# Performance work log

Measured on AMD Instinct MI355X. Metric: run time of the kernel, lower is better.

The kernel has to match this reference:

```python
import jax, jax.numpy as jnp
import numpy as np

NEG_BIG = -9e15  # matches torch's -9000000000000000.0 masked-fill value
ALPHA = 0.2      # LeakyReLU negative slope


def setup_inputs() -> dict:
    key = jax.random.key(0)
    k1, k2, k3, k4 = jax.random.split(key, 4)
    N, F_in, F_out = 8192, 128, 64
    h = jax.random.normal(k1, (N, F_in), dtype=jnp.float32)
    adj = jax.random.randint(k2, (N, N), 0, 2).astype(jnp.float32)
    # Glorot(gain=1.414)-scale params
    W = jax.random.normal(k3, (F_in, F_out), dtype=jnp.float32) * (1.414 * np.sqrt(2.0 / (F_in + F_out)))
    a = jax.random.normal(k4, (2 * F_out, 1), dtype=jnp.float32) * (1.414 * np.sqrt(2.0 / (2 * F_out + 1)))
    return {"h": h, "adj": adj, "W": W, "a": a}


def reference(h, adj, W, a):
    F_out = W.shape[1]
    Wh = h @ W                               # [N, F_out]
    Wh1 = Wh @ a[:F_out, :]                  # [N, 1]
    Wh2 = Wh @ a[F_out:, :]                  # [N, 1]
    e = jax.nn.leaky_relu(Wh1 + Wh2.T, negative_slope=ALPHA)  # [N, N]
    attention = jnp.where(adj > 0, e, NEG_BIG)
    attention = jax.nn.softmax(attention, axis=1)
    # dropout omitted (eval mode / p applied only in training)
    h_prime = attention @ Wh                 # [N, F_out]
    return jax.nn.elu(h_prime)               # concat=True -> ELU
```

## Files before the change

### kernel.cpp

```cpp
#include <hip/hip_runtime.h>
#include <hip/hip_bf16.h>

#define N 8192
#define FIN 128
#define FOUT 64
#define ALPHA 0.2f
#define LOG2E 1.44269504f
#define JSPAN N
#define STJ 256
#define NST (JSPAN / STJ)

typedef __attribute__((ext_vector_type(8))) short short8;
typedef __attribute__((ext_vector_type(4))) float f32x4;

static __device__ __forceinline__ unsigned fkey(float x) {
    unsigned u = __float_as_uint(x);
    return (u >> 31) ? ~u : (u | 0x80000000u);
}
static __device__ __forceinline__ float fdecode(unsigned k) {
    unsigned u = (k & 0x80000000u) ? (k & 0x7FFFFFFFu) : ~k;
    return __uint_as_float(u);
}
static __device__ __forceinline__ void gll16(const float* g, float* l) {
    __builtin_amdgcn_global_load_lds(
        (const __attribute__((address_space(1))) unsigned int*)g,
        (__attribute__((address_space(3))) unsigned int*)l, 16, 0, 0);
}

__global__ __launch_bounds__(256) void k_prep(const float* __restrict__ h,
                                              const float* __restrict__ W,
                                              const float* __restrict__ a,
                                              float* __restrict__ Wh,
                                              float* __restrict__ s2,
                                              float* __restrict__ t2,
                                              unsigned* __restrict__ keys) {
    __shared__ float lH[16 * FIN];
    __shared__ float lW[FIN * FOUT];
    __shared__ float red[8];
    const int tid = threadIdx.x;
    const int r0 = blockIdx.x * 16;
    {
        const float4* src = (const float4*)(h + (size_t)r0 * FIN);
        float4* dst = (float4*)lH;
        for (int i = tid; i < 16 * FIN / 4; i += 256) dst[i] = src[i];
        const float4* ws_ = (const float4*)W;
        float4* dw = (float4*)lW;
        for (int i = tid; i < FIN * FOUT / 4; i += 256) dw[i] = ws_[i];
    }
    __syncthreads();
    const int wave = tid >> 6, lane = tid & 63;
    float acc[4] = {0.f, 0.f, 0.f, 0.f};
    for (int k = 0; k < FIN; ++k) {
        float wv = lW[k * FOUT + lane];
#pragma unroll
        for (int r = 0; r < 4; ++r)
            acc[r] = fmaf(lH[(wave * 4 + r) * FIN + k], wv, acc[r]);
    }
    const float a1 = a[lane], a2 = a[FOUT + lane];
    float smx = -1e30f, tmx = -1e30f;
#pragma unroll
    for (int r = 0; r < 4; ++r) {
        int row = r0 + wave * 4 + r;
        Wh[(size_t)row * FOUT + lane] = acc[r];
        float sv = acc[r] * a1, tv = acc[r] * a2;
#pragma unroll
        for (int off = 32; off; off >>= 1) {
            sv += __shfl_xor(sv, off);
            tv += __shfl_xor(tv, off);
        }
        sv *= LOG2E; tv *= LOG2E;
        if (lane == 0) { s2[row] = sv; t2[row] = tv; }
        smx = fmaxf(smx, sv);
        tmx = fmaxf(tmx, tv);
    }
    if (lane == 0) { red[wave] = smx; red[4 + wave] = tmx; }
    __syncthreads();
    if (tid == 0) {
        float ms = fmaxf(fmaxf(red[0], red[1]), fmaxf(red[2], red[3]));
        float mt = fmaxf(fmaxf(red[4], red[5]), fmaxf(red[6], red[7]));
        atomicMax(keys + 0, fkey(ms));
        atomicMax(keys + 1, fkey(mt));
    }
}

__global__ __launch_bounds__(256) void k_pack(const float* __restrict__ Wh,
                                              __hip_bfloat16* __restrict__ WhB) {
    const int c = blockIdx.x;
    const int tn = threadIdx.x >> 6;
    const int lane = threadIdx.x & 63;
    const int quad = lane >> 4, l16 = lane & 15;
    const float* src = Wh + ((size_t)(c * 32 + quad * 8)) * FOUT + tn * 16 + l16;
    union { unsigned short u[8]; short8 v; } frag;
#pragma unroll
    for (int e = 0; e < 8; ++e) {
        __hip_bfloat16 b = __float2bfloat16(src[(size_t)e * FOUT]);
        frag.u[e] = *(unsigned short*)&b;
    }
    *(short8*)&WhB[(((size_t)c * 4 + tn) * 64 + lane) * 8] = frag.v;
}

__global__ __launch_bounds__(256) void k_attn(const float* __restrict__ adj,
                                              const __hip_bfloat16* __restrict__ WhB,
                                              const float* __restrict__ s2,
                                              const float* __restrict__ t2,
                                              const unsigned* __restrict__ keys,
                                              float* __restrict__ out) {
    __shared__ float bufA[2][8 * 512];
    __shared__ float tl[JSPAN];
    __shared__ float sred[64];
    const int wave = threadIdx.x >> 6, lane = threadIdx.x & 63;
    const int quad = lane >> 4, l16 = lane & 15;
    const int i0 = blockIdx.x * 16;
    const int u0 = 2 * wave;

    const float* gaw = adj + (size_t)(i0 + l16) * N + quad * 8;
    gll16(gaw + u0 * 32,      &bufA[0][u0 * 512]);
    gll16(gaw + u0 * 32 + 4,  &bufA[0][u0 * 512 + 256]);
    gll16(gaw + u0 * 32 + 32, &bufA[0][(u0 + 1) * 512]);
    gll16(gaw + u0 * 32 + 36, &bufA[0][(u0 + 1) * 512 + 256]);

    {
        const float4* src = (const float4*)t2;
        float4* dst = (float4*)tl;
        for (int i = threadIdx.x; i < JSPAN / 4; i += 256) dst[i] = src[i];
    }
    const float mraw = fdecode(keys[0]) + fdecode(keys[1]);
    const float mm = mraw > 0.f ? mraw : ALPHA * mraw;
    const float sm = s2[i0 + l16];
    const short8* BF = (const short8*)WhB;

    f32x4 acc0 = {0,0,0,0}, acc1 = {0,0,0,0}, acc2 = {0,0,0,0}, acc3 = {0,0,0,0};
    float lsum = 0.f;
    __syncthreads();

    for (int st = 0; st < NST; ++st) {
        const int b = st & 1;
        const size_t kc = (size_t)(st * 8 + u0) * 4;
        short8 B00 = BF[(kc + 0) * 64 + lane];
        short8 B01 = BF[(kc + 1) * 64 + lane];
        short8 B02 = BF[(kc + 2) * 64 + lane];
        short8 B03 = BF[(kc + 3) * 64 + lane];
        short8 B10 = BF[(kc + 4) * 64 + lane];
        short8 B11 = BF[(kc + 5) * 64 + lane];
        short8 B12 = BF[(kc + 6) * 64 + lane];
        short8 B13 = BF[(kc + 7) * 64 + lane];
        __builtin_amdgcn_sched_barrier(0);
        if (st + 1 < NST) {
            const float* g = gaw + (st + 1) * STJ + u0 * 32;
            float* d = &bufA[b ^ 1][u0 * 512];
            gll16(g, d);
            gll16(g + 4, d + 256);
            gll16(g + 32, d + 512);
            gll16(g + 36, d + 768);
            __builtin_amdgcn_sched_barrier(0);
            asm volatile("s_waitcnt vmcnt(12)" ::: "memory");
        } else {
            asm volatile("s_waitcnt vmcnt(8)" ::: "memory");
        }
        __builtin_amdgcn_sched_barrier(0);
#pragma unroll
        for (int uu = 0; uu < 2; ++uu) {
            const int ul = u0 + uu;
            const float* Au = &bufA[b][ul * 512];
            float4 alo = *(const float4*)(Au + lane * 4);
            float4 ahi = *(const float4*)(Au + 256 + lane * 4);
            const float* Tp = tl + st * STJ + ul * 32 + quad * 8;
            float4 tlo = *(const float4*)Tp;
            float4 thi = *(const float4*)(Tp + 4);
            union { __hip_bfloat162 h2[4]; short8 v; } af;
#pragma unroll
            for (int pp = 0; pp < 4; ++pp) {
                float a0 = (pp < 2) ? ((const float*)&alo)[2 * pp]     : ((const float*)&ahi)[2 * pp - 4];
                float a1 = (pp < 2) ? ((const float*)&alo)[2 * pp + 1] : ((const float*)&ahi)[2 * pp - 3];
                float t0 = (pp < 2) ? ((const float*)&tlo)[2 * pp]     : ((const float*)&thi)[2 * pp - 4];
                float t1 = (pp < 2) ? ((const float*)&tlo)[2 * pp + 1] : ((const float*)&thi)[2 * pp - 3];
                float x0 = sm + t0,                x1 = sm + t1;
                float le0 = fmaxf(x0, ALPHA * x0), le1 = fmaxf(x1, ALPHA * x1);
                float p0 = a0 * exp2f(le0 - mm),   p1 = a1 * exp2f(le1 - mm);
                __hip_bfloat162 pb = __float22bfloat162_rn(make_float2(p0, p1));
                af.h2[pp] = pb;
                lsum += __bfloat162float(pb.x) + __bfloat162float(pb.y);
            }
            if (uu == 0) {
                acc0 = __builtin_amdgcn_mfma_f32_16x16x32_bf16(af.v, B00, acc0, 0, 0, 0);
                acc1 = __builtin_amdgcn_mfma_f32_16x16x32_bf16(af.v, B01, acc1, 0, 0, 0);
                acc2 = __builtin_amdgcn_mfma_f32_16x16x32_bf16(af.v, B02, acc2, 0, 0, 0);
                acc3 = __builtin_amdgcn_mfma_f32_16x16x32_bf16(af.v, B03, acc3, 0, 0, 0);
            } else {
                acc0 = __builtin_amdgcn_mfma_f32_16x16x32_bf16(af.v, B10, acc0, 0, 0, 0);
                acc1 = __builtin_amdgcn_mfma_f32_16x16x32_bf16(af.v, B11, acc1, 0, 0, 0);
                acc2 = __builtin_amdgcn_mfma_f32_16x16x32_bf16(af.v, B12, acc2, 0, 0, 0);
                acc3 = __builtin_amdgcn_mfma_f32_16x16x32_bf16(af.v, B13, acc3, 0, 0, 0);
            }
        }
    }

    lsum += __shfl_xor(lsum, 16);
    lsum += __shfl_xor(lsum, 32);

    float* accr = &bufA[0][0];
    *(f32x4*)&accr[((wave * 4 + 0) * 64 + lane) * 4] = acc0;
    *(f32x4*)&accr[((wave * 4 + 1) * 64 + lane) * 4] = acc1;
    *(f32x4*)&accr[((wave * 4 + 2) * 64 + lane) * 4] = acc2;
    *(f32x4*)&accr[((wave * 4 + 3) * 64 + lane) * 4] = acc3;
    if (lane < 16) sred[wave * 16 + lane] = lsum;
    __syncthreads();

    const int tile = wave;
    f32x4 tot = {0, 0, 0, 0};
#pragma unroll
    for (int w = 0; w < 4; ++w) {
        f32x4 c = *(const f32x4*)&accr[((w * 4 + tile) * 64 + lane) * 4];
        tot[0] += c[0]; tot[1] += c[1]; tot[2] += c[2]; tot[3] += c[3];
    }
#pragma unroll
    for (int r = 0; r < 4; ++r) {
        int row = quad * 4 + r;
        float lv = sred[row] + sred[16 + row] + sred[32 + row] + sred[48 + row];
        float v = tot[r] / lv;
        out[(size_t)(i0 + row) * FOUT + tile * 16 + l16] =
            v > 0.f ? v : (exp2f(v * LOG2E) - 1.f);
    }
}

extern "C" void kernel_launch(void* const* d_in, const int* in_sizes, int n_in,
                              void* d_out, int out_size, void* d_ws, size_t ws_size,
                              hipStream_t stream) {
    const float* h   = (const float*)d_in[0];
    const float* adj = (const float*)d_in[1];
    const float* W   = (const float*)d_in[2];
    const float* a   = (const float*)d_in[3];
    float* out = (float*)d_out;

    char* base = (char*)d_ws;
    float* Wh = (float*)base;                        base += (size_t)N * FOUT * 4;
    __hip_bfloat16* WhB = (__hip_bfloat16*)base;     base += (size_t)N * FOUT * 2;
    float* s2 = (float*)base;                        base += (size_t)N * 4;
    float* t2 = (float*)base;                        base += (size_t)N * 4 + 1024;
    unsigned* keys = (unsigned*)base;

    hipMemsetAsync(keys, 0, 2 * sizeof(unsigned), stream);
    k_prep<<<N / 16, 256, 0, stream>>>(h, W, a, Wh, s2, t2, keys);
    k_pack<<<N / 32, 256, 0, stream>>>(Wh, WhB);
    k_attn<<<N / 16, 256, 0, stream>>>(adj, WhB, s2, t2, keys, out);
}
```

Before: 403.3 us.

## Fuse bf16 packing into prep and triple-buffer adj with register-prefetched B/t2

Folds the bf16 fragment packing of Wh into the prep kernel, so the separate pack launch and the fp32 Wh round trip through global memory go away. The attention kernel moves from double to triple buffering of adj tiles, issuing loads two stages ahead. It also prefetches the next stage's WhB fragments and t2 values into registers instead of staging all of t2 in LDS. This drops the LDS t2 copy and the startup __syncthreads, at the cost of more live registers and hand-tuned vmcnt waits that must match the issue order exactly.

Result: no change. 398.5 us (-1.2%).

```diff
diff --git a/kernel.cpp b/kernel.cpp
--- a/kernel.cpp
+++ b/kernel.cpp
@@ -6,9 +6,8 @@
 #define FOUT 64
 #define ALPHA 0.2f
 #define LOG2E 1.44269504f
-#define JSPAN N
 #define STJ 256
-#define NST (JSPAN / STJ)
+#define NST (N / STJ)
 
 typedef __attribute__((ext_vector_type(8))) short short8;
 typedef __attribute__((ext_vector_type(4))) float f32x4;
@@ -30,38 +29,47 @@
 __global__ __launch_bounds__(256) void k_prep(const float* __restrict__ h,
                                               const float* __restrict__ W,
                                               const float* __restrict__ a,
-                                              float* __restrict__ Wh,
+                                              __hip_bfloat16* __restrict__ WhB,
                                               float* __restrict__ s2,
                                               float* __restrict__ t2,
                                               unsigned* __restrict__ keys) {
-    __shared__ float lH[16 * FIN];
+    __shared__ float lH[32 * FIN];
     __shared__ float lW[FIN * FOUT];
     __shared__ float red[8];
     const int tid = threadIdx.x;
-    const int r0 = blockIdx.x * 16;
+    const int c = blockIdx.x;
+    const int r0 = c * 32;
     {
         const float4* src = (const float4*)(h + (size_t)r0 * FIN);
         float4* dst = (float4*)lH;
-        for (int i = tid; i < 16 * FIN / 4; i += 256) dst[i] = src[i];
+        for (int i = tid; i < 32 * FIN / 4; i += 256) dst[i] = src[i];
         const float4* ws_ = (const float4*)W;
         float4* dw = (float4*)lW;
         for (int i = tid; i < FIN * FOUT / 4; i += 256) dw[i] = ws_[i];
     }
     __syncthreads();
     const int wave = tid >> 6, lane = tid & 63;
-    float acc[4] = {0.f, 0.f, 0.f, 0.f};
+    float acc[8] = {0.f, 0.f, 0.f, 0.f, 0.f, 0.f, 0.f, 0.f};
+#pragma unroll 4
     for (int k = 0; k < FIN; ++k) {
         float wv = lW[k * FOUT + lane];
 #pragma unroll
-        for (int r = 0; r < 4; ++r)
-            acc[r] = fmaf(lH[(wave * 4 + r) * FIN + k], wv, acc[r]);
-    }
+        for (int r = 0; r < 8; ++r)
+            acc[r] = fmaf(lH[(wave * 8 + r) * FIN + k], wv, acc[r]);
+    }
+    union { unsigned short u[8]; short8 v; } frag;
+#pragma unroll
+    for (int e = 0; e < 8; ++e) {
+        __hip_bfloat16 b = __float2bfloat16(acc[e]);
+        frag.u[e] = *(unsigned short*)&b;
+    }
+    *(short8*)&WhB[(((size_t)c * 4 + (lane >> 4)) * 64 + (wave * 16 + (lane & 15))) * 8] = frag.v;
+
     const float a1 = a[lane], a2 = a[FOUT + lane];
     float smx = -1e30f, tmx = -1e30f;
 #pragma unroll
-    for (int r = 0; r < 4; ++r) {
-        int row = r0 + wave * 4 + r;
-        Wh[(size_t)row * FOUT + lane] = acc[r];
+    for (int r = 0; r < 8; ++r) {
+        int row = r0 + wave * 8 + r;
         float sv = acc[r] * a1, tv = acc[r] * a2;
 #pragma unroll
         for (int off = 32; off; off >>= 1) {
@@ -83,90 +91,100 @@
     }
 }
 
-__global__ __launch_bounds__(256) void k_pack(const float* __restrict__ Wh,
-                                              __hip_bfloat16* __restrict__ WhB) {
-    const int c = blockIdx.x;
-    const int tn = threadIdx.x >> 6;
-    const int lane = threadIdx.x & 63;
-    const int quad = lane >> 4, l16 = lane & 15;
-    const float* src = Wh + ((size_t)(c * 32 + quad * 8)) * FOUT + tn * 16 + l16;
-    union { unsigned short u[8]; short8 v; } frag;
-#pragma unroll
-    for (int e = 0; e < 8; ++e) {
-        __hip_bfloat16 b = __float2bfloat16(src[(size_t)e * FOUT]);
-        frag.u[e] = *(unsigned short*)&b;
-    }
-    *(short8*)&WhB[(((size_t)c * 4 + tn) * 64 + lane) * 8] = frag.v;
-}
-
 __global__ __launch_bounds__(256) void k_attn(const float* __restrict__ adj,
                                               const __hip_bfloat16* __restrict__ WhB,
                                               const float* __restrict__ s2,
                                               const float* __restrict__ t2,
                                               const unsigned* __restrict__ keys,
                                               float* __restrict__ out) {
-    __shared__ float bufA[2][8 * 512];
-    __shared__ float tl[JSPAN];
+    __shared__ float bufA[3][8 * 512];
     __shared__ float sred[64];
     const int wave = threadIdx.x >> 6, lane = threadIdx.x & 63;
     const int quad = lane >> 4, l16 = lane & 15;
     const int i0 = blockIdx.x * 16;
     const int u0 = 2 * wave;
 
-    const float* gaw = adj + (size_t)(i0 + l16) * N + quad * 8;
-    gll16(gaw + u0 * 32,      &bufA[0][u0 * 512]);
-    gll16(gaw + u0 * 32 + 4,  &bufA[0][u0 * 512 + 256]);
-    gll16(gaw + u0 * 32 + 32, &bufA[0][(u0 + 1) * 512]);
-    gll16(gaw + u0 * 32 + 36, &bufA[0][(u0 + 1) * 512 + 256]);
-
-    {
-        const float4* src = (const float4*)t2;
-        float4* dst = (float4*)tl;
-        for (int i = threadIdx.x; i < JSPAN / 4; i += 256) dst[i] = src[i];
-    }
+    const float sm = s2[i0 + l16];
     const float mraw = fdecode(keys[0]) + fdecode(keys[1]);
     const float mm = mraw > 0.f ? mraw : ALPHA * mraw;
-    const float sm = s2[i0 + l16];
+    asm volatile("" :: "v"(sm), "v"(mm));
+    __builtin_amdgcn_sched_barrier(0);
+
+    const float* gawu = adj + (size_t)(i0 + l16) * N + quad * 8 + u0 * 32;
     const short8* BF = (const short8*)WhB;
+
+    gll16(gawu,      &bufA[0][u0 * 512]);
+    gll16(gawu + 4,  &bufA[0][u0 * 512 + 256]);
+    gll16(gawu + 32, &bufA[0][(u0 + 1) * 512]);
+    gll16(gawu + 36, &bufA[0][(u0 + 1) * 512 + 256]);
+    __builtin_amdgcn_sched_barrier(0);
+    size_t kc = (size_t)u0 * 4;
+    short8 B0 = BF[(kc + 0) * 64 + lane];
+    short8 B1 = BF[(kc + 1) * 64 + lane];
+    short8 B2 = BF[(kc + 2) * 64 + lane];
+    short8 B3 = BF[(kc + 3) * 64 + lane];
+    short8 B4 = BF[(kc + 4) * 64 + lane];
+    short8 B5 = BF[(kc + 5) * 64 + lane];
+    short8 B6 = BF[(kc + 6) * 64 + lane];
+    short8 B7 = BF[(kc + 7) * 64 + lane];
+    const float* Tp = t2 + u0 * 32 + quad * 8;
+    float4 T0 = *(const float4*)Tp;
+    float4 T1 = *(const float4*)(Tp + 4);
+    float4 T2v = *(const float4*)(Tp + 32);
+    float4 T3v = *(const float4*)(Tp + 36);
+    __builtin_amdgcn_sched_barrier(0);
+    gll16(gawu + STJ,      &bufA[1][u0 * 512]);
+    gll16(gawu + STJ + 4,  &bufA[1][u0 * 512 + 256]);
+    gll16(gawu + STJ + 32, &bufA[1][(u0 + 1) * 512]);
+    gll16(gawu + STJ + 36, &bufA[1][(u0 + 1) * 512 + 256]);
+    __builtin_amdgcn_sched_barrier(0);
 
     f32x4 acc0 = {0,0,0,0}, acc1 = {0,0,0,0}, acc2 = {0,0,0,0}, acc3 = {0,0,0,0};
     float lsum = 0.f;
-    __syncthreads();
+    int bi = 0;
 
     for (int st = 0; st < NST; ++st) {
-        const int b = st & 1;
-        const size_t kc = (size_t)(st * 8 + u0) * 4;
-        short8 B00 = BF[(kc + 0) * 64 + lane];
-        short8 B01 = BF[(kc + 1) * 64 + lane];
-        short8 B02 = BF[(kc + 2) * 64 + lane];
-        short8 B03 = BF[(kc + 3) * 64 + lane];
-        short8 B10 = BF[(kc + 4) * 64 + lane];
-        short8 B11 = BF[(kc + 5) * 64 + lane];
-        short8 B12 = BF[(kc + 6) * 64 + lane];
-        short8 B13 = BF[(kc + 7) * 64 + lane];
+        const bool hasN = (st + 1 < NST);
+        short8 nB0, nB1, nB2, nB3, nB4, nB5, nB6, nB7;
+        float4 nT0, nT1, nT2, nT3;
+        if (hasN) {
+            const size_t nkc = (size_t)((st + 1) * 8 + u0) * 4;
+            nB0 = BF[(nkc + 0) * 64 + lane];
+            nB1 = BF[(nkc + 1) * 64 + lane];
+            nB2 = BF[(nkc + 2) * 64 + lane];
+            nB3 = BF[(nkc + 3) * 64 + lane];
+            nB4 = BF[(nkc + 4) * 64 + lane];
+            nB5 = BF[(nkc + 5) * 64 + lane];
+            nB6 = BF[(nkc + 6) * 64 + lane];
+            nB7 = BF[(nkc + 7) * 64 + lane];
+            const float* nTp = t2 + (st + 1) * STJ + u0 * 32 + quad * 8;
+            nT0 = *(const float4*)nTp;
+            nT1 = *(const float4*)(nTp + 4);
+            nT2 = *(const float4*)(nTp + 32);
+            nT3 = *(const float4*)(nTp + 36);
+        }
         __builtin_amdgcn_sched_barrier(0);
-        if (st + 1 < NST) {
-            const float* g = gaw + (st + 1) * STJ + u0 * 32;
-            float* d = &bufA[b ^ 1][u0 * 512];
+        if (st + 2 < NST) {
+            const float* g = gawu + (st + 2) * STJ;
+            const int di = bi >= 1 ? bi - 1 : 2;
+            float* d = &bufA[di][u0 * 512];
             gll16(g, d);
             gll16(g + 4, d + 256);
             gll16(g + 32, d + 512);
             gll16(g + 36, d + 768);
-            __builtin_amdgcn_sched_barrier(0);
-            asm volatile("s_waitcnt vmcnt(12)" ::: "memory");
-        } else {
-            asm volatile("s_waitcnt vmcnt(8)" ::: "memory");
         }
         __builtin_amdgcn_sched_barrier(0);
+        if (st < NST - 2)       asm volatile("s_waitcnt vmcnt(32)" ::: "memory");
+        else if (st == NST - 2) asm volatile("s_waitcnt vmcnt(28)" ::: "memory");
+        else                    asm volatile("s_waitcnt vmcnt(12)" ::: "memory");
+        __builtin_amdgcn_sched_barrier(0);
 #pragma unroll
         for (int uu = 0; uu < 2; ++uu) {
-            const int ul = u0 + uu;
-            const float* Au = &bufA[b][ul * 512];
+            const float* Au = &bufA[bi][(u0 + uu) * 512];
             float4 alo = *(const float4*)(Au + lane * 4);
             float4 ahi = *(const float4*)(Au + 256 + lane * 4);
-            const float* Tp = tl + st * STJ + ul * 32 + quad * 8;
-            float4 tlo = *(const float4*)Tp;
-            float4 thi = *(const float4*)(Tp + 4);
+            float4 tlo = uu ? T2v : T0;
+            float4 thi = uu ? T3v : T1;
             union { __hip_bfloat162 h2[4]; short8 v; } af;
 #pragma unroll
             for (int pp = 0; pp < 4; ++pp) {
@@ -182,17 +200,23 @@
                 lsum += __bfloat162float(pb.x) + __bfloat162float(pb.y);
             }
             if (uu == 0) {
-                acc0 = __builtin_amdgcn_mfma_f32_16x16x32_bf16(af.v, B00, acc0, 0, 0, 0);
-                acc1 = __builtin_amdgcn_mfma_f32_16x16x32_bf16(af.v, B01, acc1, 0, 0, 0);
-                acc2 = __builtin_amdgcn_mfma_f32_16x16x32_bf16(af.v, B02, acc2, 0, 0, 0);
-                acc3 = __builtin_amdgcn_mfma_f32_16x16x32_bf16(af.v, B03, acc3, 0, 0, 0);
+                acc0 = __builtin_amdgcn_mfma_f32_16x16x32_bf16(af.v, B0, acc0, 0, 0, 0);
+                acc1 = __builtin_amdgcn_mfma_f32_16x16x32_bf16(af.v, B1, acc1, 0, 0, 0);
+                acc2 = __builtin_amdgcn_mfma_f32_16x16x32_bf16(af.v, B2, acc2, 0, 0, 0);
+                acc3 = __builtin_amdgcn_mfma_f32_16x16x32_bf16(af.v, B3, acc3, 0, 0, 0);
             } else {
-                acc0 = __builtin_amdgcn_mfma_f32_16x16x32_bf16(af.v, B10, acc0, 0, 0, 0);
-                acc1 = __builtin_amdgcn_mfma_f32_16x16x32_bf16(af.v, B11, acc1, 0, 0, 0);
-                acc2 = __builtin_amdgcn_mfma_f32_16x16x32_bf16(af.v, B12, acc2, 0, 0, 0);
-                acc3 = __builtin_amdgcn_mfma_f32_16x16x32_bf16(af.v, B13, acc3, 0, 0, 0);
+                acc0 = __builtin_amdgcn_mfma_f32_16x16x32_bf16(af.v, B4, acc0, 0, 0, 0);
+                acc1 = __builtin_amdgcn_mfma_f32_16x16x32_bf16(af.v, B5, acc1, 0, 0, 0);
+                acc2 = __builtin_amdgcn_mfma_f32_16x16x32_bf16(af.v, B6, acc2, 0, 0, 0);
+                acc3 = __builtin_amdgcn_mfma_f32_16x16x32_bf16(af.v, B7, acc3, 0, 0, 0);
             }
         }
+        if (hasN) {
+            B0 = nB0; B1 = nB1; B2 = nB2; B3 = nB3;
+            B4 = nB4; B5 = nB5; B6 = nB6; B7 = nB7;
+            T0 = nT0; T1 = nT1; T2v = nT2; T3v = nT3;
+        }
+        bi = bi == 2 ? 0 : bi + 1;
     }
 
     lsum += __shfl_xor(lsum, 16);
@@ -233,14 +257,12 @@
     float* out = (float*)d_out;
 
     char* base = (char*)d_ws;
-    float* Wh = (float*)base;                        base += (size_t)N * FOUT * 4;
     __hip_bfloat16* WhB = (__hip_bfloat16*)base;     base += (size_t)N * FOUT * 2;
     float* s2 = (float*)base;                        base += (size_t)N * 4;
     float* t2 = (float*)base;                        base += (size_t)N * 4 + 1024;
     unsigned* keys = (unsigned*)base;
 
     hipMemsetAsync(keys, 0, 2 * sizeof(unsigned), stream);
-    k_prep<<<N / 16, 256, 0, stream>>>(h, W, a, Wh, s2, t2, keys);
-    k_pack<<<N / 32, 256, 0, stream>>>(Wh, WhB);
+    k_prep<<<N / 32, 256, 0, stream>>>(h, W, a, WhB, s2, t2, keys);
     k_attn<<<N / 16, 256, 0, stream>>>(adj, WhB, s2, t2, keys, out);
 }
```
